# Kernel tuning notes

Hardware: AMD Instinct MI355X
Metric: run time of the kernel (lower is better)

The kernel has to match this reference:

```python
import jax, jax.numpy as jnp
import numpy as np

N = 50000   # num nodes
E = 800000  # num edges (before self loops)
D = 64      # embed_dim (in == out)
R = 16      # num_relations
EPS = 1e-9


def setup_inputs() -> dict:
    key = jax.random.key(0)
    ks = jax.random.split(key, 8)
    xavier = float(np.sqrt(6.0 / (D + D)))  # xavier_uniform bound for [D, D] fans
    return {
        "x": jax.random.normal(ks[0], (N, D), dtype=jnp.float32),
        "edge_index": jax.random.randint(ks[1], (2, E), 0, N),
        # edge attrs sized E + N to cover self loops added in forward
        "edge_type": jax.random.randint(ks[2], (E + N,), 0, R),
        "path_length": jax.random.uniform(ks[3], (E + N,), jnp.float32, 1.0, 8.0),
        "rel_weight1": jax.random.uniform(ks[4], (R, D, D), jnp.float32, -xavier, xavier),
        "bias1": jnp.zeros((D,), jnp.float32),
        "rel_weight2": jax.random.uniform(ks[5], (R, D, D), jnp.float32, -xavier, xavier),
        "bias2": jnp.zeros((D,), jnp.float32),
        "num_nodes": N,
    }


def _conv(x, src, dst, edge_type, path_length, rel_weight, bias, num_nodes):
    # gather relation-specific weights per edge: [E', D, D]
    w = rel_weight[edge_type]
    # per-edge matvec: x_j @ W_rel -> [E', D]
    msg = jnp.einsum("ei,eio->eo", x[src], w)
    msg = msg / jnp.clip(path_length, EPS, None)[:, None]
    # scatter-add to destination nodes
    aggr = jax.ops.segment_sum(msg, dst, num_segments=num_nodes)
    return jax.nn.relu(aggr + bias)


def reference(x, edge_index, edge_type, path_length, rel_weight1, bias1,
              rel_weight2, bias2, num_nodes):
    loops = jnp.arange(num_nodes)
    src = jnp.concatenate([edge_index[0], loops])  # x_j source (flow src->dst)
    dst = jnp.concatenate([edge_index[1], loops])
    x = _conv(x, src, dst, edge_type, path_length, rel_weight1, bias1, num_nodes)
    x = _conv(x, src, dst, edge_type, path_length, rel_weight2, bias2, num_nodes)
    return x
```

## Files before the change

### kernel.cpp

```cpp
#include <hip/hip_runtime.h>

#define DD 64
#define RR 16
#define EPSF 1e-9f
#define BINCH 4096

typedef unsigned short ushort_t;
typedef __bf16 bf16x8 __attribute__((ext_vector_type(8)));
typedef float f32x4 __attribute__((ext_vector_type(4)));
union F8 { uint4 u; bf16x8 v; };

__device__ __forceinline__ void fma4(float4& a, const float4& w, float s) {
    a.x = fmaf(w.x, s, a.x); a.y = fmaf(w.y, s, a.y);
    a.z = fmaf(w.z, s, a.z); a.w = fmaf(w.w, s, a.w);
}
__device__ __forceinline__ unsigned f2bf(float f) {
    unsigned u = __float_as_uint(f);
    return (u + 0x7FFFu + ((u >> 16) & 1u)) >> 16;
}
__device__ __forceinline__ uint2 pk4(float4 v) {
    return make_uint2(f2bf(v.x) | (f2bf(v.y) << 16),
                      f2bf(v.z) | (f2bf(v.w) << 16));
}
__device__ __forceinline__ float bf_lo(unsigned u) { return __uint_as_float(u << 16); }
__device__ __forceinline__ float bf_hi(unsigned u) { return __uint_as_float(u & 0xFFFF0000u); }

__device__ __forceinline__ void packW_one(
    const float* __restrict__ W, ushort_t* __restrict__ Wb, int t)
{
    int lane = t & 63;
    int ot = (t >> 6) & 3;
    int kb = (t >> 8) & 1;
    int r  = t >> 9;
    int o  = ot * 16 + (lane & 15);
    int k0 = kb * 32 + (lane >> 4) * 8;
    const float* w = W + ((size_t)r * DD + k0) * DD + o;
    unsigned d[4];
    #pragma unroll
    for (int p = 0; p < 4; ++p)
        d[p] = f2bf(w[(2 * p) * DD]) | (f2bf(w[(2 * p + 1) * DD]) << 16);
    ((uint4*)Wb)[t] = make_uint4(d[0], d[1], d[2], d[3]);
}

__global__ __launch_bounds__(256) void k_prep(
    const float* __restrict__ W1, const float* __restrict__ W2,
    ushort_t* __restrict__ Wb1, ushort_t* __restrict__ Wb2,
    int* __restrict__ cursor, int B, int cap)
{
    int tid = blockIdx.x * 256 + threadIdx.x;
    if (tid < 8192)            packW_one(W1, Wb1, tid);
    else if (tid < 16384)      packW_one(W2, Wb2, tid - 8192);
    else if (tid - 16384 < B)  cursor[tid - 16384] = (tid - 16384) * cap;
}

__global__ __launch_bounds__(256) void k_bin(
    const int* __restrict__ ei, const int* __restrict__ et,
    const float* __restrict__ pl, int* __restrict__ cursor,
    uint2* __restrict__ ep, int E, int B, int N, int cap)
{
    __shared__ int hl[1024];
    __shared__ int bl[1024];
    for (int i = threadIdx.x; i < B; i += 256) hl[i] = 0;
    __syncthreads();
    const int e0 = blockIdx.x * BINCH;
    #pragma unroll 4
    for (int k = 0; k < BINCH / 256; ++k) {
        int e = e0 + k * 256 + threadIdx.x;
        if (e < E) atomicAdd(&hl[ei[E + e] >> 6], 1);
    }
    __syncthreads();
    for (int i = threadIdx.x; i < B; i += 256) {
        int c = hl[i];
        bl[i] = c ? atomicAdd(&cursor[i], c) : 0;
        hl[i] = 0;
    }
    __syncthreads();
    #pragma unroll 2
    for (int k = 0; k < BINCH / 256; ++k) {
        int e = e0 + k * 256 + threadIdx.x;
        if (e < E) {
            int dst = ei[E + e];
            int b = dst >> 6;
            int rank = atomicAdd(&hl[b], 1);
            int pos = bl[b] + rank;
            if (pos < (b + 1) * cap) {
                int idx = et[e] * N + ei[e];
                float iv = 1.0f / fmaxf(pl[e], EPSF);
                ep[pos] = make_uint2((unsigned)idx | ((unsigned)(dst & 63) << 20),
                                     __float_as_uint(iv));
            }
        }
    }
}

__global__ __launch_bounds__(256) void k_sortb(
    const uint2* __restrict__ ep, const int* __restrict__ cursor,
    uint2* __restrict__ ep2, int* __restrict__ rp, int B, int cap)
{
    __shared__ int hist[64];
    __shared__ int off[64];
    const int b = blockIdx.x, tid = threadIdx.x;
    const int beg = b * cap;
    int cnt = cursor[b] - beg;
    if (cnt > cap) cnt = cap;
    const int end = beg + cnt;
    if (tid < 64) hist[tid] = 0;
    __syncthreads();
    for (int p = beg + tid; p < end; p += 256)
        atomicAdd(&hist[(ep[p].x >> 20) & 63u], 1);
    __syncthreads();
    if (tid == 0) {
        int run = 0;
        #pragma unroll
        for (int i = 0; i < 64; ++i) { off[i] = run; run += hist[i]; }
    }
    __syncthreads();
    if (tid < 64) {
        rp[b * 65 + tid] = beg + off[tid];
        hist[tid] = 0;
    }
    if (tid == 64) rp[b * 65 + 64] = end;
    __syncthreads();
    for (int p = beg + tid; p < end; p += 256) {
        uint2 m = ep[p];
        int d = (m.x >> 20) & 63u;
        int rank = atomicAdd(&hist[d], 1);
        ep2[beg + off[d] + rank] = make_uint2(m.x & 0xFFFFFu, m.y);
    }
}

__global__ __launch_bounds__(256) void k_transform_mfma(
    const float* __restrict__ x, const ushort_t* __restrict__ Wb,
    ushort_t* __restrict__ Y, int N)
{
    const int lane = threadIdx.x & 63;
    const int m0 = (blockIdx.x * 4 + (threadIdx.x >> 6)) * 16;
    if (m0 >= N) return;
    const int quad = lane >> 4, c = lane & 15;

    int node = m0 + c; if (node >= N) node = N - 1;
    const float* xr = x + (size_t)node * DD + quad * 8;
    float4 xa = *(const float4*)xr;
    float4 xb = *(const float4*)(xr + 4);
    float4 xc = *(const float4*)(xr + 32);
    float4 xd = *(const float4*)(xr + 36);
    F8 a0, a1;
    { uint2 p = pk4(xa), q = pk4(xb); a0.u = make_uint4(p.x, p.y, q.x, q.y); }
    { uint2 p = pk4(xc), q = pk4(xd); a1.u = make_uint4(p.x, p.y, q.x, q.y); }

    const uint4* wbp = (const uint4*)Wb + lane;
    const bool full = (m0 + 16 <= N);

    for (int r = 0; r < RR; ++r) {
        ushort_t* yr = Y + ((size_t)r * N + m0) * DD + c;
        #pragma unroll
        for (int ot = 0; ot < 4; ++ot) {
            F8 b0, b1;
            b0.u = wbp[(size_t)(r * 8 + ot) * 64];
            b1.u = wbp[(size_t)(r * 8 + 4 + ot) * 64];
            f32x4 acc = {0.f, 0.f, 0.f, 0.f};
            acc = __builtin_amdgcn_mfma_f32_16x16x32_bf16(a0.v, b0.v, acc, 0, 0, 0);
            acc = __builtin_amdgcn_mfma_f32_16x16x32_bf16(a1.v, b1.v, acc, 0, 0, 0);
            ushort_t* yp = yr + (ot << 4);
            if (full) {
                #pragma unroll
                for (int g = 0; g < 4; ++g)
                    yp[(size_t)(quad * 4 + g) * DD] = (ushort_t)f2bf(acc[g]);
            } else {
                #pragma unroll
                for (int g = 0; g < 4; ++g)
                    if (m0 + quad * 4 + g < N)
                        yp[(size_t)(quad * 4 + g) * DD] = (ushort_t)f2bf(acc[g]);
            }
        }
    }
}

__global__ __launch_bounds__(256) void k_aggregate(
    const ushort_t* __restrict__ Y, const int* __restrict__ rp,
    const uint2* __restrict__ ep,
    const int* __restrict__ et, const float* __restrict__ pl,
    const float* __restrict__ bias, float* __restrict__ out, int N, int E)
{
    const int n = blockIdx.x * 8 + (threadIdx.x >> 5);
    const int lane = threadIdx.x & 31;
    if (n >= N) return;
    const int b = n >> 6, i = n & 63;
    const int beg = rp[b * 65 + i], end = rp[b * 65 + i + 1];

    int rts = et[E + n];
    float ivs = 1.0f / fmaxf(pl[E + n], EPSF);
    unsigned yv = *(const unsigned*)(Y + (size_t)(rts * N + n) * DD + 2 * lane);

    float accx = 0.f, accy = 0.f;
    for (int p0 = beg; p0 < end; p0 += 32) {
        int cnt = end - p0; if (cnt > 32) cnt = 32;
        unsigned pk = 0, ivb = 0;
        if (lane < cnt) { uint2 m = ep[p0 + lane]; pk = m.x; ivb = m.y; }
        for (int jj = 0; jj < cnt; jj += 8) {
            unsigned v[8]; float ivv[8];
            #pragma unroll
            for (int q = 0; q < 8; ++q) {
                int t = (jj + q) & 31;
                unsigned pkj = (unsigned)__shfl((int)pk, t, 32);
                float iv = __uint_as_float((unsigned)__shfl((int)ivb, t, 32));
                ivv[q] = (jj + q < cnt) ? iv : 0.f;
                v[q] = *(const unsigned*)(Y + (size_t)(pkj & 0xFFFFFu) * DD + 2 * lane);
            }
            #pragma unroll
            for (int q = 0; q < 8; ++q) {
                accx = fmaf(bf_lo(v[q]), ivv[q], accx);
                accy = fmaf(bf_hi(v[q]), ivv[q], accy);
            }
        }
    }
    accx = fmaf(bf_lo(yv), ivs, accx);
    accy = fmaf(bf_hi(yv), ivs, accy);

    float2 bb = *(const float2*)(bias + 2 * lane);
    float2 o;
    o.x = fmaxf(accx + bb.x, 0.f);
    o.y = fmaxf(accy + bb.y, 0.f);
    *(float2*)(out + (size_t)n * DD + 2 * lane) = o;
}

__global__ __launch_bounds__(256) void k_transform(
    const float* __restrict__ x, const float* __restrict__ W,
    ushort_t* __restrict__ Y, int N, int r_base, int r_cnt, int yr_off)
{
    __shared__ float xt[DD * 128];
    __shared__ float ws[DD * DD];
    const int n0 = blockIdx.x * 128;
    const int tid = threadIdx.x;

    #pragma unroll
    for (int c = 0; c < 8; ++c) {
        int idx = c * 256 + tid;
        int n  = idx >> 4;
        int i4 = (idx & 15) << 2;
        int gn = n0 + n;
        float4 v = make_float4(0.f, 0.f, 0.f, 0.f);
        if (gn < N) v = ((const float4*)(x + (size_t)gn * DD))[idx & 15];
        int n4 = n >> 2, nr = n & 3;
        float vv[4] = {v.x, v.y, v.z, v.w};
        #pragma unroll
        for (int k = 0; k < 4; ++k) {
            int i = i4 + k;
            int swz = (i >> 2) & 7;
            xt[i * 128 + (((n4 ^ swz) << 2) | nr)] = vv[k];
        }
    }

    const int j  = tid & 15;
    const int nq = tid >> 4;

    for (int rr = 0; rr < r_cnt; ++rr) {
        const int r = r_base + blockIdx.y * r_cnt + rr;
        __syncthreads();
        {
            const float4* Wv = (const float4*)(W + (size_t)r * DD * DD);
            float4* wv = (float4*)ws;
            #pragma unroll
            for (int c = 0; c < 4; ++c) wv[c * 256 + tid] = Wv[c * 256 + tid];
        }
        __syncthreads();

        float4 acc[8];
        #pragma unroll
        for (int m = 0; m < 8; ++m) acc[m] = make_float4(0.f, 0.f, 0.f, 0.f);

        #pragma unroll 4
        for (int i = 0; i < DD; ++i) {
            const int swz = (i >> 2) & 7;
            const float4 wv = *(const float4*)&ws[i * DD + 4 * j];
            #pragma unroll
            for (int h = 0; h < 2; ++h) {
                const int col4 = (2 * nq + h) ^ swz;
                const float4 xv = *(const float4*)&xt[i * 128 + (col4 << 2)];
                fma4(acc[4 * h + 0], wv, xv.x);
                fma4(acc[4 * h + 1], wv, xv.y);
                fma4(acc[4 * h + 2], wv, xv.z);
                fma4(acc[4 * h + 3], wv, xv.w);
            }
        }

        const size_t ybase = (size_t)(r - yr_off) * N;
        #pragma unroll
        for (int m = 0; m < 8; ++m) {
            int node = n0 + 8 * nq + 4 * (m >> 2) + (m & 3);
            if (node < N)
                *(uint2*)(Y + (ybase + node) * DD + 4 * j) = pk4(acc[m]);
        }
    }
}

__global__ __launch_bounds__(256) void k_edges(
    const int* __restrict__ ei, const int* __restrict__ et,
    const float* __restrict__ pl, const ushort_t* __restrict__ Y,
    float* __restrict__ aggr, int N, int E, int Etot, int rel_filter)
{
    int sub = threadIdx.x >> 5;
    int lane = threadIdx.x & 31;
    int e = blockIdx.x * 8 + sub;
    if (e >= Etot) return;
    int rt = et[e];
    int yrel = rt;
    if (rel_filter >= 0) { if (rt != rel_filter) return; yrel = 0; }
    int src, dst;
    if (e < E) { src = ei[e]; dst = ei[E + e]; }
    else       { src = dst = e - E; }
    float inv = 1.0f / fmaxf(pl[e], EPSF);
    unsigned v = *(const unsigned*)(Y + ((size_t)yrel * N + src) * DD + 2 * lane);
    atomicAdd(&aggr[(size_t)dst * DD + 2 * lane],     bf_lo(v) * inv);
    atomicAdd(&aggr[(size_t)dst * DD + 2 * lane + 1], bf_hi(v) * inv);
}

__global__ __launch_bounds__(256) void k_bias_relu(
    const float* __restrict__ aggr, const float* __restrict__ bias,
    float* __restrict__ out, int N)
{
    int idx = blockIdx.x * 256 + threadIdx.x;
    if (idx >= N * (DD / 4)) return;
    float4 a = ((const float4*)aggr)[idx];
    int o4 = (idx & 15) * 4;
    a.x = fmaxf(a.x + bias[o4 + 0], 0.f);
    a.y = fmaxf(a.y + bias[o4 + 1], 0.f);
    a.z = fmaxf(a.z + bias[o4 + 2], 0.f);
    a.w = fmaxf(a.w + bias[o4 + 3], 0.f);
    ((float4*)out)[idx] = a;
}

__global__ __launch_bounds__(256) void k_zero(float* __restrict__ p, size_t n)
{
    size_t i = (size_t)blockIdx.x * 256 + threadIdx.x;
    size_t stride = (size_t)gridDim.x * 256;
    for (; i < n; i += stride) p[i] = 0.f;
}

extern "C" void kernel_launch(void* const* d_in, const int* in_sizes, int n_in,
                              void* d_out, int out_size, void* d_ws, size_t ws_size,
                              hipStream_t stream)
{
    const float* x  = (const float*)d_in[0];
    const int*   ei = (const int*)d_in[1];
    const int*   et = (const int*)d_in[2];
    const float* pl = (const float*)d_in[3];
    const float* W1 = (const float*)d_in[4];
    const float* b1 = (const float*)d_in[5];
    const float* W2 = (const float*)d_in[6];
    const float* b2 = (const float*)d_in[7];
    float* out = (float*)d_out;

    const int N = in_sizes[0] / DD;
    const int E = in_sizes[1] / 2;
    const size_t ndf = (size_t)N * DD;
    const size_t wb_elems = (size_t)RR * 2 * 4 * 64 * 8;
    const int B = (N + 63) / 64;

    int avg = (E + B - 1) / B;
    int cap = avg + 8 * (int)sqrtf((float)avg) + 64;
    cap = (cap + 3) & ~3;

    char* wsb = (char*)d_ws;
    ushort_t* Y   = (ushort_t*)wsb;
    float* aggr1  = (float*)(wsb + (size_t)RR * ndf * 2);
    ushort_t* Wb1 = (ushort_t*)((char*)aggr1 + ndf * 4);
    ushort_t* Wb2 = Wb1 + wb_elems;
    uint2* ep     = (uint2*)(Wb2 + wb_elems);
    uint2* ep2    = ep + (size_t)B * cap;
    int* cursor   = (int*)(ep2 + (size_t)B * cap);
    int* rp       = cursor + B;

    const size_t need_main = (size_t)RR * ndf * 2 + ndf * 4 + wb_elems * 4 +
        (size_t)B * cap * 16 + ((size_t)B * 66) * 4;
    const bool main_ok = (ws_size >= need_main) && (N <= 65535) && (B <= 1024);

    if (main_ok) {
        const int gBin = (E + BINCH - 1) / BINCH;
        k_prep<<<(16384 + B + 255) / 256, 256, 0, stream>>>(W1, W2, Wb1, Wb2,
                                                            cursor, B, cap);
        k_bin<<<gBin, 256, 0, stream>>>(ei, et, pl, cursor, ep, E, B, N, cap);
        k_sortb<<<B, 256, 0, stream>>>(ep, cursor, ep2, rp, B, cap);

        const int gT = (N + 63) / 64;
        const int gA = (N + 7) / 8;
        for (int layer = 0; layer < 2; ++layer) {
            const float* xin   = layer ? aggr1 : x;
            const ushort_t* Wb = layer ? Wb2 : Wb1;
            const float* bias  = layer ? b2 : b1;
            float* dest        = layer ? out : aggr1;
            k_transform_mfma<<<gT, 256, 0, stream>>>(xin, Wb, Y, N);
            k_aggregate<<<gA, 256, 0, stream>>>(Y, rp, ep2, et, pl,
                                                bias, dest, N, E);
        }
        return;
    }

    ushort_t* Yc = (ushort_t*)wsb;
    float* ag    = (float*)(wsb + ndf * 2);
    const int gx     = (N + 127) / 128;
    const int gEdgeT = (E + N + 7) / 8;
    const int gQuad  = (N * (DD / 4) + 255) / 256;
    float* hid = ag;

    for (int layer = 0; layer < 2; ++layer) {
        const float* xin  = layer ? hid : x;
        const float* W    = layer ? W2 : W1;
        const float* bias = layer ? b2 : b1;
        float* aggr       = layer ? out : ag;
        k_zero<<<1024, 256, 0, stream>>>(aggr, ndf);
        for (int r = 0; r < RR; ++r) {
            k_transform<<<dim3(gx, 1), 256, 0, stream>>>(xin, W, Yc, N, r, 1, r);
            k_edges<<<gEdgeT, 256, 0, stream>>>(ei, et, pl, Yc, aggr, N, E, E + N, r);
        }
        k_bias_relu<<<gQuad, 256, 0, stream>>>(aggr, bias, layer ? out : hid, N);
    }
}
```

Baseline: 221.8 us.

## Fold self-loop edges into binned edge lists and use 16-lane aggregation

```diff
diff --git a/kernel.cpp b/kernel.cpp
--- a/kernel.cpp
+++ b/kernel.cpp
@@ -45,12 +45,25 @@
 __global__ __launch_bounds__(256) void k_prep(
     const float* __restrict__ W1, const float* __restrict__ W2,
     ushort_t* __restrict__ Wb1, ushort_t* __restrict__ Wb2,
-    int* __restrict__ cursor, int B, int cap)
+    int* __restrict__ cursor, uint2* __restrict__ ep,
+    const int* __restrict__ et, const float* __restrict__ pl,
+    int B, int cap, int N, int E)
 {
     int tid = blockIdx.x * 256 + threadIdx.x;
     if (tid < 8192)            packW_one(W1, Wb1, tid);
     else if (tid < 16384)      packW_one(W2, Wb2, tid - 8192);
-    else if (tid - 16384 < B)  cursor[tid - 16384] = (tid - 16384) * cap;
+    else if (tid < 16384 + B) {
+        int b = tid - 16384;
+        int nb = N - b * 64; if (nb > 64) nb = 64;
+        cursor[b] = b * cap + nb;
+    } else if (tid < 16384 + B + N) {
+        int n = tid - 16384 - B;
+        int b = n >> 6;
+        int idx = et[E + n] * N + n;
+        float iv = 1.0f / fmaxf(pl[E + n], EPSF);
+        ep[(size_t)b * cap + (n & 63)] = make_uint2(
+            (unsigned)idx | ((unsigned)(n & 63) << 20), __float_as_uint(iv));
+    }
 }
 
 __global__ __launch_bounds__(256) void k_bin(
@@ -179,49 +192,45 @@
 __global__ __launch_bounds__(256) void k_aggregate(
     const ushort_t* __restrict__ Y, const int* __restrict__ rp,
     const uint2* __restrict__ ep,
-    const int* __restrict__ et, const float* __restrict__ pl,
-    const float* __restrict__ bias, float* __restrict__ out, int N, int E)
-{
-    const int n = blockIdx.x * 8 + (threadIdx.x >> 5);
-    const int lane = threadIdx.x & 31;
+    const float* __restrict__ bias, float* __restrict__ out, int N)
+{
+    const int n = blockIdx.x * 16 + (threadIdx.x >> 4);
+    const int l = threadIdx.x & 15;
     if (n >= N) return;
     const int b = n >> 6, i = n & 63;
     const int beg = rp[b * 65 + i], end = rp[b * 65 + i + 1];
 
-    int rts = et[E + n];
-    float ivs = 1.0f / fmaxf(pl[E + n], EPSF);
-    unsigned yv = *(const unsigned*)(Y + (size_t)(rts * N + n) * DD + 2 * lane);
-
-    float accx = 0.f, accy = 0.f;
-    for (int p0 = beg; p0 < end; p0 += 32) {
-        int cnt = end - p0; if (cnt > 32) cnt = 32;
+    float a0 = 0.f, a1 = 0.f, a2 = 0.f, a3 = 0.f;
+    for (int p0 = beg; p0 < end; p0 += 16) {
+        int cnt = end - p0; if (cnt > 16) cnt = 16;
         unsigned pk = 0, ivb = 0;
-        if (lane < cnt) { uint2 m = ep[p0 + lane]; pk = m.x; ivb = m.y; }
+        if (l < cnt) { uint2 m = ep[p0 + l]; pk = m.x; ivb = m.y; }
         for (int jj = 0; jj < cnt; jj += 8) {
-            unsigned v[8]; float ivv[8];
+            uint2 v[8]; float ivv[8];
             #pragma unroll
             for (int q = 0; q < 8; ++q) {
-                int t = (jj + q) & 31;
-                unsigned pkj = (unsigned)__shfl((int)pk, t, 32);
-                float iv = __uint_as_float((unsigned)__shfl((int)ivb, t, 32));
+                int t = (jj + q) & 15;
+                unsigned pkj = (unsigned)__shfl((int)pk, t, 16);
+                float iv = __uint_as_float((unsigned)__shfl((int)ivb, t, 16));
                 ivv[q] = (jj + q < cnt) ? iv : 0.f;
-                v[q] = *(const unsigned*)(Y + (size_t)(pkj & 0xFFFFFu) * DD + 2 * lane);
+                v[q] = *(const uint2*)(Y + (size_t)pkj * DD + 4 * l);
             }
             #pragma unroll
             for (int q = 0; q < 8; ++q) {
-                accx = fmaf(bf_lo(v[q]), ivv[q], accx);
-                accy = fmaf(bf_hi(v[q]), ivv[q], accy);
+                a0 = fmaf(bf_lo(v[q].x), ivv[q], a0);
+                a1 = fmaf(bf_hi(v[q].x), ivv[q], a1);
+                a2 = fmaf(bf_lo(v[q].y), ivv[q], a2);
+                a3 = fmaf(bf_hi(v[q].y), ivv[q], a3);
             }
         }
     }
-    accx = fmaf(bf_lo(yv), ivs, accx);
-    accy = fmaf(bf_hi(yv), ivs, accy);
-
-    float2 bb = *(const float2*)(bias + 2 * lane);
-    float2 o;
-    o.x = fmaxf(accx + bb.x, 0.f);
-    o.y = fmaxf(accy + bb.y, 0.f);
-    *(float2*)(out + (size_t)n * DD + 2 * lane) = o;
+    float4 bb = *(const float4*)(bias + 4 * l);
+    float4 o;
+    o.x = fmaxf(a0 + bb.x, 0.f);
+    o.y = fmaxf(a1 + bb.y, 0.f);
+    o.z = fmaxf(a2 + bb.z, 0.f);
+    o.w = fmaxf(a3 + bb.w, 0.f);
+    *(float4*)(out + (size_t)n * DD + 4 * l) = o;
 }
 
 __global__ __launch_bounds__(256) void k_transform(
@@ -358,7 +367,7 @@
     const int B = (N + 63) / 64;
 
     int avg = (E + B - 1) / B;
-    int cap = avg + 8 * (int)sqrtf((float)avg) + 64;
+    int cap = avg + 8 * (int)sqrtf((float)avg) + 128;
     cap = (cap + 3) & ~3;
 
     char* wsb = (char*)d_ws;
@@ -377,21 +386,20 @@
 
     if (main_ok) {
         const int gBin = (E + BINCH - 1) / BINCH;
-        k_prep<<<(16384 + B + 255) / 256, 256, 0, stream>>>(W1, W2, Wb1, Wb2,
-                                                            cursor, B, cap);
+        k_prep<<<(16384 + B + N + 255) / 256, 256, 0, stream>>>(
+            W1, W2, Wb1, Wb2, cursor, ep, et, pl, B, cap, N, E);
         k_bin<<<gBin, 256, 0, stream>>>(ei, et, pl, cursor, ep, E, B, N, cap);
         k_sortb<<<B, 256, 0, stream>>>(ep, cursor, ep2, rp, B, cap);
 
         const int gT = (N + 63) / 64;
-        const int gA = (N + 7) / 8;
+        const int gA = (N + 15) / 16;
         for (int layer = 0; layer < 2; ++layer) {
             const float* xin   = layer ? aggr1 : x;
             const ushort_t* Wb = layer ? Wb2 : Wb1;
             const float* bias  = layer ? b2 : b1;
             float* dest        = layer ? out : aggr1;
             k_transform_mfma<<<gT, 256, 0, stream>>>(xin, Wb, Y, N);
-            k_aggregate<<<gA, 256, 0, stream>>>(Y, rp, ep2, et, pl,
-                                                bias, dest, N, E);
+            k_aggregate<<<gA, 256, 0, stream>>>(Y, rp, ep2, bias, dest, N);
         }
         return;
     }
```

New measurement: 227.8 us. 1.03x slower.

## Fold self-loop edges into binned edge list and stage edge attrs in LDS

Applied to the files above, without the earlier changes.

```diff
diff --git a/kernel.cpp b/kernel.cpp
--- a/kernel.cpp
+++ b/kernel.cpp
@@ -45,12 +45,25 @@
 __global__ __launch_bounds__(256) void k_prep(
     const float* __restrict__ W1, const float* __restrict__ W2,
     ushort_t* __restrict__ Wb1, ushort_t* __restrict__ Wb2,
-    int* __restrict__ cursor, int B, int cap)
+    int* __restrict__ cursor, uint2* __restrict__ ep,
+    const int* __restrict__ et, const float* __restrict__ pl,
+    int B, int cap, int N, int E)
 {
     int tid = blockIdx.x * 256 + threadIdx.x;
     if (tid < 8192)            packW_one(W1, Wb1, tid);
     else if (tid < 16384)      packW_one(W2, Wb2, tid - 8192);
-    else if (tid - 16384 < B)  cursor[tid - 16384] = (tid - 16384) * cap;
+    else if (tid < 16384 + B) {
+        int b = tid - 16384;
+        int nb = N - b * 64; if (nb > 64) nb = 64;
+        cursor[b] = b * cap + nb;
+    } else if (tid < 16384 + B + N) {
+        int n = tid - 16384 - B;
+        int b = n >> 6;
+        int idx = et[E + n] * N + n;
+        float iv = 1.0f / fmaxf(pl[E + n], EPSF);
+        ep[(size_t)b * cap + (n & 63)] = make_uint2(
+            (unsigned)idx | ((unsigned)(n & 63) << 20), __float_as_uint(iv));
+    }
 }
 
 __global__ __launch_bounds__(256) void k_bin(
@@ -60,13 +73,23 @@
 {
     __shared__ int hl[1024];
     __shared__ int bl[1024];
+    __shared__ unsigned lkey[BINCH];
+    __shared__ unsigned ldst[BINCH];
+    __shared__ float    liv[BINCH];
     for (int i = threadIdx.x; i < B; i += 256) hl[i] = 0;
     __syncthreads();
     const int e0 = blockIdx.x * BINCH;
     #pragma unroll 4
     for (int k = 0; k < BINCH / 256; ++k) {
-        int e = e0 + k * 256 + threadIdx.x;
-        if (e < E) atomicAdd(&hl[ei[E + e] >> 6], 1);
+        int i = k * 256 + threadIdx.x;
+        int e = e0 + i;
+        if (e < E) {
+            int dst = ei[E + e];
+            atomicAdd(&hl[dst >> 6], 1);
+            lkey[i] = (unsigned)(et[e] * N + ei[e]);
+            ldst[i] = (unsigned)dst;
+            liv[i]  = 1.0f / fmaxf(pl[e], EPSF);
+        }
     }
     __syncthreads();
     for (int i = threadIdx.x; i < B; i += 256) {
@@ -77,18 +100,16 @@
     __syncthreads();
     #pragma unroll 2
     for (int k = 0; k < BINCH / 256; ++k) {
-        int e = e0 + k * 256 + threadIdx.x;
+        int i = k * 256 + threadIdx.x;
+        int e = e0 + i;
         if (e < E) {
-            int dst = ei[E + e];
+            unsigned dst = ldst[i];
             int b = dst >> 6;
             int rank = atomicAdd(&hl[b], 1);
             int pos = bl[b] + rank;
-            if (pos < (b + 1) * cap) {
-                int idx = et[e] * N + ei[e];
-                float iv = 1.0f / fmaxf(pl[e], EPSF);
-                ep[pos] = make_uint2((unsigned)idx | ((unsigned)(dst & 63) << 20),
-                                     __float_as_uint(iv));
-            }
+            if (pos < (b + 1) * cap)
+                ep[pos] = make_uint2(lkey[i] | ((dst & 63u) << 20),
+                                     __float_as_uint(liv[i]));
         }
     }
 }
@@ -109,14 +130,15 @@
     for (int p = beg + tid; p < end; p += 256)
         atomicAdd(&hist[(ep[p].x >> 20) & 63u], 1);
     __syncthreads();
-    if (tid == 0) {
-        int run = 0;
+    if (tid < 64) {
+        int v = hist[tid], s = v;
         #pragma unroll
-        for (int i = 0; i < 64; ++i) { off[i] = run; run += hist[i]; }
-    }
-    __syncthreads();
-    if (tid < 64) {
-        rp[b * 65 + tid] = beg + off[tid];
+        for (int o = 1; o < 64; o <<= 1) {
+            int t = __shfl_up(s, o, 64);
+            if (tid >= o) s += t;
+        }
+        off[tid] = s - v;
+        rp[b * 65 + tid] = beg + s - v;
         hist[tid] = 0;
     }
     if (tid == 64) rp[b * 65 + 64] = end;
@@ -179,18 +201,13 @@
 __global__ __launch_bounds__(256) void k_aggregate(
     const ushort_t* __restrict__ Y, const int* __restrict__ rp,
     const uint2* __restrict__ ep,
-    const int* __restrict__ et, const float* __restrict__ pl,
-    const float* __restrict__ bias, float* __restrict__ out, int N, int E)
+    const float* __restrict__ bias, float* __restrict__ out, int N)
 {
     const int n = blockIdx.x * 8 + (threadIdx.x >> 5);
     const int lane = threadIdx.x & 31;
     if (n >= N) return;
     const int b = n >> 6, i = n & 63;
     const int beg = rp[b * 65 + i], end = rp[b * 65 + i + 1];
-
-    int rts = et[E + n];
-    float ivs = 1.0f / fmaxf(pl[E + n], EPSF);
-    unsigned yv = *(const unsigned*)(Y + (size_t)(rts * N + n) * DD + 2 * lane);
 
     float accx = 0.f, accy = 0.f;
     for (int p0 = beg; p0 < end; p0 += 32) {
@@ -214,9 +231,6 @@
             }
         }
     }
-    accx = fmaf(bf_lo(yv), ivs, accx);
-    accy = fmaf(bf_hi(yv), ivs, accy);
-
     float2 bb = *(const float2*)(bias + 2 * lane);
     float2 o;
     o.x = fmaxf(accx + bb.x, 0.f);
@@ -358,7 +372,7 @@
     const int B = (N + 63) / 64;
 
     int avg = (E + B - 1) / B;
-    int cap = avg + 8 * (int)sqrtf((float)avg) + 64;
+    int cap = avg + 8 * (int)sqrtf((float)avg) + 128;
     cap = (cap + 3) & ~3;
 
     char* wsb = (char*)d_ws;
@@ -377,8 +391,8 @@
 
     if (main_ok) {
         const int gBin = (E + BINCH - 1) / BINCH;
-        k_prep<<<(16384 + B + 255) / 256, 256, 0, stream>>>(W1, W2, Wb1, Wb2,
-                                                            cursor, B, cap);
+        k_prep<<<(16384 + B + N + 255) / 256, 256, 0, stream>>>(
+            W1, W2, Wb1, Wb2, cursor, ep, et, pl, B, cap, N, E);
         k_bin<<<gBin, 256, 0, stream>>>(ei, et, pl, cursor, ep, E, B, N, cap);
         k_sortb<<<B, 256, 0, stream>>>(ep, cursor, ep2, rp, B, cap);
 
@@ -390,8 +404,7 @@
             const float* bias  = layer ? b2 : b1;
             float* dest        = layer ? out : aggr1;
             k_transform_mfma<<<gT, 256, 0, stream>>>(xin, Wb, Y, N);
-            k_aggregate<<<gA, 256, 0, stream>>>(Y, rp, ep2, et, pl,
-                                                bias, dest, N, E);
+            k_aggregate<<<gA, 256, 0, stream>>>(Y, rp, ep2, bias, dest, N);
         }
         return;
     }
```

New measurement: 219.3 us. About the same (-1.1%).
